# Kernel tuning notes

Measured on AMD Instinct MI355X. Metric: run time of the kernel, lower is better.

The kernel has to match this reference:

```python
import jax, jax.numpy as jnp
import numpy as np


def _apply_ring(x, angles):
    """Apply x @ R^T where R = G_0 @ G_1 @ ... @ G_{n-1} with ring planes
    (k, (k+1) % n). Equivalent to applying G_k^T to x for k = n-1 .. 0:
      x[:, k] <- c*x[:, k] - s*x[:, j]
      x[:, j] <- s*x[:, k] + c*x[:, j]
    x: [B, n], angles: [n].
    """
    n = angles.shape[0]

    def step(xT, k):
        a = angles[k]
        c, s = jnp.cos(a), jnp.sin(a)
        j = jnp.mod(k + 1, n)
        xi = xT[k]
        xj = xT[j]
        xT = xT.at[k].set(c * xi - s * xj)
        xT = xT.at[j].set(s * xi + c * xj)
        return xT, None

    ks = jnp.arange(n - 1, -1, -1)  # reverse order: R^T = G_{n-1}^T ... G_0^T
    xT, _ = jax.lax.scan(step, x.T, ks)  # carry is [n, B]
    return xT.T


def setup_inputs() -> dict:
    key = jax.random.key(0)
    k_x, k_e, k_d = jax.random.split(key, 3)
    B, n, num_blocks = 8192, 1024, 4
    return {
        "x": jax.random.normal(k_x, (B, n), dtype=jnp.float32),
        "angles_enc": jax.random.normal(k_e, (num_blocks, n), dtype=jnp.float32),
        "angles_dec": jax.random.normal(k_d, (num_blocks, n), dtype=jnp.float32),
        "hidden_weight": jnp.zeros((1,), dtype=jnp.float32),
        "hidden_state": jnp.zeros((n,), dtype=jnp.float32),
    }


def reference(x, angles_enc, angles_dec, hidden_weight, hidden_state):
    num_blocks = angles_enc.shape[0]
    b = x
    for blk in range(num_blocks):
        b = _apply_ring(b, angles_enc[blk])
    # recurrent blend; weight uses the detached hidden_weight (original uses
    # numpy on .detach()), so stop_gradient matches the original semantics.
    w = jax.nn.sigmoid(jax.lax.stop_gradient(hidden_weight[0]))
    bottleneck = (1.0 - w) * b + w * hidden_state[None, :]
    out = bottleneck
    for blk in range(num_blocks):
        out = _apply_ring(out, angles_dec[blk])
    return (bottleneck, out)
```

## Files before the change

### kernel.cpp

```cpp
#include <hip/hip_runtime.h>
#include <math.h>

#define N_COLS 1024
#define NRINGS 8

#define TPR    32
#define CHUNK  32
#define ROWS_PER_BLOCK 8

#define F_OFF   16384
#define A_OFF   24576
#define AUX_OFF 24832
#define WS_FLOATS 24848

__global__ void ced_setup(const float* __restrict__ ae,
                          const float* __restrict__ ad,
                          float* __restrict__ ws)
{
    __shared__ float2 ls[N_COLS];
    const int r   = blockIdx.x;
    const int tid = threadIdx.x;
    const float* ang = (r < 4) ? (ae + (r << 10)) : (ad + ((r - 4) << 10));

    #pragma unroll
    for (int m = 0; m < 4; ++m) {
        int k = tid * 4 + m;
        float sv, cv;
        sincosf(ang[k], &sv, &cv);
        if (k == N_COLS - 1) {
            ((float2*)(ws + AUX_OFF))[r] = make_float2(cv, sv);
            cv = 0.f; sv = -1.f;
        }
        ls[k] = make_float2(cv, sv);
    }
    __syncthreads();

    {
        int k0 = tid * 4;
        int t  = k0 >> 5;
        int jp = (k0 & 31) >> 1;
        float4* CS = (float4*)ws;
        float2 e0 = ls[k0], e1 = ls[k0+1], e2 = ls[k0+2], e3 = ls[k0+3];
        CS[(r*16 + jp    )*32 + t] = make_float4(e0.x, e0.y, e1.x, e1.y);
        CS[(r*16 + jp + 1)*32 + t] = make_float4(e2.x, e2.y, e3.x, e3.y);
    }

    if (tid < TPR) {
        int t = tid;
        float f[CHUNK];
        float P = 1.f;
        for (int j = CHUNK - 1; j >= 0; --j) {
            float2 cs = ls[t*CHUNK + j];
            f[j] = cs.x * P;
            P    = -cs.y * P;
        }
        float4* F = (float4*)(ws + F_OFF);
        #pragma unroll
        for (int qi = 0; qi < 8; ++qi)
            F[(r*8 + qi)*32 + t] = make_float4(f[4*qi], f[4*qi+1], f[4*qi+2], f[4*qi+3]);
        ws[A_OFF + r*TPR + t] = P;
    }
}

__global__ __launch_bounds__(256, 4)
void ced_main(const float* __restrict__ x,
              const float* __restrict__ ws,
              const float* __restrict__ hw,
              const float* __restrict__ hs,
              float* __restrict__ out, int B)
{
    const float4* CS  = (const float4*)ws;
    const float4* F   = (const float4*)(ws + F_OFF);
    const float*  A   = ws + A_OFF;
    const float2* AUX = (const float2*)(ws + AUX_OFF);

    const int tid  = threadIdx.x;
    const int lane = tid & 63;
    const int t    = lane & 31;
    const int g    = lane >> 5;
    const int groupBase = lane & 32;
    const int row  = blockIdx.x * ROWS_PER_BLOCK + (tid >> 6) * 2 + g;

    float y[CHUNK];
    const float4* xp = (const float4*)(x + (size_t)row * N_COLS + t * CHUNK);
    #pragma unroll
    for (int i = 0; i < 8; ++i) {
        float4 v = xp[i];
        y[4*i] = v.x; y[4*i+1] = v.y; y[4*i+2] = v.z; y[4*i+3] = v.w;
    }

    const float w   = 1.f / (1.f + expf(-hw[0]));
    const float omw = 1.f - w;

    #pragma unroll 1
    for (int r = 0; r < NRINGS; ++r) {
        if (r == 4) {
            float4* ob = (float4*)(out + (size_t)row * N_COLS + t * CHUNK);
            const float4* hp = (const float4*)(hs + t * CHUNK);
            #pragma unroll
            for (int i = 0; i < 8; ++i) {
                float4 h = hp[i];
                float4 bn;
                bn.x = fmaf(omw, y[4*i+0], w * h.x);
                bn.y = fmaf(omw, y[4*i+1], w * h.y);
                bn.z = fmaf(omw, y[4*i+2], w * h.z);
                bn.w = fmaf(omw, y[4*i+3], w * h.w);
                ob[i] = bn;
                y[4*i+0] = bn.x; y[4*i+1] = bn.y; y[4*i+2] = bn.z; y[4*i+3] = bn.w;
            }
        }

        const float2 cN = AUX[r];
        float y0 = __shfl(y[0],       groupBase);
        float yN = __shfl(y[CHUNK-1], groupBase + 31);
        float Cinit = cN.x * yN - cN.y * y0;
        float x0n   = fmaf(cN.y, yN, cN.x * y0);
        if (t == 0) y[0] = x0n;

        float carry = 0.f, ztmp = 0.f;
        const float4* csr = CS + r * 512 + t;
        #pragma unroll
        for (int jp = CHUNK/2 - 1; jp >= 0; --jp) {
            float4 cs4 = csr[jp * 32];
            const int j1 = 2*jp + 1;
            float z1 = fmaf(cs4.w, y[j1], cs4.z * carry);
            carry    = fmaf(-cs4.w, carry, cs4.z * y[j1]);
            if (j1 == CHUNK - 1) ztmp = z1; else y[j1+1] = z1;
            const int j0 = 2*jp;
            float z0s = fmaf(cs4.y, y[j0], cs4.x * carry);
            carry     = fmaf(-cs4.y, carry, cs4.x * y[j0]);
            y[j0+1] = z0s;
        }

        float sa = A[r*32 + t];
        float sb = carry;
        #pragma unroll
        for (int d = 1; d < TPR; d <<= 1) {
            float a2 = __shfl_down(sa, d);
            float b2 = __shfl_down(sb, d);
            if (t + d < TPR) { sb = fmaf(sa, b2, sb); sa *= a2; }
        }
        float ea = __shfl_down(sa, 1), eb = __shfl_down(sb, 1);
        float zfirst = fmaf(sa, Cinit, sb);
        float Cin = (t == TPR - 1) ? Cinit : fmaf(ea, Cinit, eb);

        const float4* fr = F + r * 256 + t;
        #pragma unroll
        for (int qi = CHUNK/4 - 1; qi >= 0; --qi) {
            float4 f4 = fr[qi * 32];
            const int j = 4*qi;
            if (j + 3 == CHUNK - 1) ztmp   = fmaf(f4.w, Cin, ztmp);
            else                    y[j+4] = fmaf(f4.w, Cin, y[j+4]);
            y[j+3] = fmaf(f4.z, Cin, y[j+3]);
            y[j+2] = fmaf(f4.y, Cin, y[j+2]);
            y[j+1] = fmaf(f4.x, Cin, y[j+1]);
        }

        float up = __shfl_up(ztmp, 1);
        y[0] = (t == 0) ? zfirst : up;
    }

    float4* oo = (float4*)(out + (size_t)B * N_COLS + (size_t)row * N_COLS + t * CHUNK);
    #pragma unroll
    for (int i = 0; i < 8; ++i)
        oo[i] = make_float4(y[4*i], y[4*i+1], y[4*i+2], y[4*i+3]);
}

__global__ __launch_bounds__(256, 2)
void ced_fallback(const float* __restrict__ x,
                  const float* __restrict__ ae,
                  const float* __restrict__ ad,
                  const float* __restrict__ hw,
                  const float* __restrict__ hs,
                  float* __restrict__ out, int B)
{
    __shared__ float2 s_cs[NRINGS * 64 * 16];
    __shared__ float  s_A [NRINGS * 16];
    __shared__ float2 s_aux[NRINGS];

    const int tid = threadIdx.x;
    for (int i = 0; i < 32; ++i) {
        int idx = i * 256 + tid;
        int r   = idx >> 10;
        int k   = idx & 1023;
        const float* ang = (r < 4) ? (ae + (r << 10)) : (ad + ((r - 4) << 10));
        float sv, cv;
        sincosf(ang[k], &sv, &cv);
        int t = k >> 6, j = k & 63;
        float2 e = make_float2(cv, sv);
        if (k == 1023) { s_aux[r] = e; e = make_float2(0.f, -1.f); }
        s_cs[(r * 64 + j) * 16 + t] = e;
    }
    __syncthreads();
    if (tid < NRINGS * 16) {
        int r = tid >> 4, t = tid & 15;
        float p = 1.f;
        for (int j = 0; j < 64; ++j) p *= -s_cs[(r * 64 + j) * 16 + t].y;
        s_A[tid] = p;
    }
    __syncthreads();

    const int lane      = tid & 63;
    const int g         = lane >> 4;
    const int t         = lane & 15;
    const int groupBase = lane & 48;
    const int row       = blockIdx.x * 16 + (tid >> 6) * 4 + g;

    const float* xr = x + (size_t)row * N_COLS + t * 64;
    float y[64];
    #pragma unroll
    for (int i = 0; i < 16; ++i) {
        float4 v = ((const float4*)xr)[i];
        y[4*i] = v.x; y[4*i+1] = v.y; y[4*i+2] = v.z; y[4*i+3] = v.w;
    }
    const float w   = 1.f / (1.f + expf(-hw[0]));
    const float omw = 1.f - w;

    for (int r = 0; r < NRINGS; ++r) {
        if (r == 4) {
            float4* ob = (float4*)(out + (size_t)row * N_COLS + t * 64);
            const float4* hp = (const float4*)(hs + t * 64);
            #pragma unroll
            for (int i = 0; i < 16; ++i) {
                float4 h = hp[i];
                float4 bn;
                bn.x = fmaf(omw, y[4*i+0], w * h.x);
                bn.y = fmaf(omw, y[4*i+1], w * h.y);
                bn.z = fmaf(omw, y[4*i+2], w * h.z);
                bn.w = fmaf(omw, y[4*i+3], w * h.w);
                ob[i] = bn;
                y[4*i+0] = bn.x; y[4*i+1] = bn.y; y[4*i+2] = bn.z; y[4*i+3] = bn.w;
            }
        }
        const float2* csr = s_cs + r * 64 * 16;
        const float2  cN  = s_aux[r];
        float y0 = __shfl(y[0],  groupBase);
        float yN = __shfl(y[63], groupBase + 15);
        float Cinit = cN.x * yN - cN.y * y0;
        float x0n   = fmaf(cN.y, yN, cN.x * y0);
        if (t == 0) y[0] = x0n;

        float carry = 0.f, ztmp = 0.f;
        #pragma unroll
        for (int j = 63; j >= 0; --j) {
            float2 cs = csr[j * 16 + t];
            float z   = fmaf(cs.y, y[j], cs.x * carry);
            carry     = fmaf(-cs.y, carry, cs.x * y[j]);
            if (j == 63) ztmp = z; else y[j + 1] = z;
        }
        float sa = s_A[r * 16 + t], sb = carry;
        #pragma unroll
        for (int d = 1; d < 16; d <<= 1) {
            float a2 = __shfl_down(sa, d);
            float b2 = __shfl_down(sb, d);
            if (t + d < 16) { sb = fmaf(sa, b2, sb); sa *= a2; }
        }
        float ea = __shfl_down(sa, 1);
        float eb = __shfl_down(sb, 1);
        float z0  = fmaf(sa, Cinit, sb);
        float Cin = (t == 15) ? Cinit : fmaf(ea, Cinit, eb);

        float P = 1.f;
        #pragma unroll
        for (int j = 63; j >= 0; --j) {
            float2 cs = csr[j * 16 + t];
            float f = cs.x * P;
            P = -cs.y * P;
            if (j == 63) ztmp = fmaf(f, Cin, ztmp);
            else         y[j + 1] = fmaf(f, Cin, y[j + 1]);
        }
        float up = __shfl_up(ztmp, 1);
        y[0] = (t == 0) ? z0 : up;
    }

    float4* oo = (float4*)(out + (size_t)B * N_COLS + (size_t)row * N_COLS + t * 64);
    #pragma unroll
    for (int i = 0; i < 16; ++i)
        oo[i] = make_float4(y[4*i], y[4*i+1], y[4*i+2], y[4*i+3]);
}

extern "C" void kernel_launch(void* const* d_in, const int* in_sizes, int n_in,
                              void* d_out, int out_size, void* d_ws, size_t ws_size,
                              hipStream_t stream) {
    const float* x  = (const float*)d_in[0];
    const float* ae = (const float*)d_in[1];
    const float* ad = (const float*)d_in[2];
    const float* hw = (const float*)d_in[3];
    const float* hs = (const float*)d_in[4];
    float* out = (float*)d_out;
    const int B = in_sizes[0] / N_COLS;

    if (ws_size >= WS_FLOATS * sizeof(float)) {
        hipLaunchKernelGGL(ced_setup, dim3(NRINGS), dim3(256), 0, stream,
                           ae, ad, (float*)d_ws);
        hipLaunchKernelGGL(ced_main, dim3(B / ROWS_PER_BLOCK), dim3(256), 0, stream,
                           x, (const float*)d_ws, hw, hs, out, B);
    } else {
        hipLaunchKernelGGL(ced_fallback, dim3(B / 16), dim3(256), 0, stream,
                           x, ae, ad, hw, hs, out, B);
    }
}
```

Measured before the change: 137.3 us.

## Parallelize setup suffix-product scan and prefetch ring coefficients into registers

```diff
diff --git a/kernel.cpp b/kernel.cpp
--- a/kernel.cpp
+++ b/kernel.cpp
@@ -13,9 +13,10 @@
 #define AUX_OFF 24832
 #define WS_FLOATS 24848
 
-__global__ void ced_setup(const float* __restrict__ ae,
-                          const float* __restrict__ ad,
-                          float* __restrict__ ws)
+__global__ __launch_bounds__(256)
+void ced_setup(const float* __restrict__ ae,
+               const float* __restrict__ ad,
+               float* __restrict__ ws)
 {
     __shared__ float2 ls[N_COLS];
     const int r   = blockIdx.x;
@@ -24,7 +25,7 @@
 
     #pragma unroll
     for (int m = 0; m < 4; ++m) {
-        int k = tid * 4 + m;
+        int k = (m << 8) + tid;
         float sv, cv;
         sincosf(ang[k], &sv, &cv);
         if (k == N_COLS - 1) {
@@ -35,31 +36,33 @@
     }
     __syncthreads();
 
-    {
-        int k0 = tid * 4;
-        int t  = k0 >> 5;
-        int jp = (k0 & 31) >> 1;
-        float4* CS = (float4*)ws;
-        float2 e0 = ls[k0], e1 = ls[k0+1], e2 = ls[k0+2], e3 = ls[k0+3];
-        CS[(r*16 + jp    )*32 + t] = make_float4(e0.x, e0.y, e1.x, e1.y);
-        CS[(r*16 + jp + 1)*32 + t] = make_float4(e2.x, e2.y, e3.x, e3.y);
-    }
-
-    if (tid < TPR) {
-        int t = tid;
-        float f[CHUNK];
-        float P = 1.f;
-        for (int j = CHUNK - 1; j >= 0; --j) {
-            float2 cs = ls[t*CHUNK + j];
-            f[j] = cs.x * P;
-            P    = -cs.y * P;
-        }
-        float4* F = (float4*)(ws + F_OFF);
-        #pragma unroll
-        for (int qi = 0; qi < 8; ++qi)
-            F[(r*8 + qi)*32 + t] = make_float4(f[4*qi], f[4*qi+1], f[4*qi+2], f[4*qi+3]);
-        ws[A_OFF + r*TPR + t] = P;
-    }
+    const int t = tid >> 3;
+    const int q = tid & 7;
+    const int j0 = t * CHUNK + 4 * q;
+    float2 e0 = ls[j0], e1 = ls[j0+1], e2 = ls[j0+2], e3 = ls[j0+3];
+
+    float4* CSw = (float4*)ws;
+    CSw[(r*16 + 2*q    )*32 + t] = make_float4(e0.x, e0.y, e1.x, e1.y);
+    CSw[(r*16 + 2*q + 1)*32 + t] = make_float4(e2.x, e2.y, e3.x, e3.y);
+
+    float f3 = e3.x;       float P = -e3.y;
+    float f2 = e2.x * P;   P *= -e2.y;
+    float f1 = e1.x * P;   P *= -e1.y;
+    float f0 = e0.x * P;   P *= -e0.y;
+
+    float ip = P;
+    #pragma unroll
+    for (int d = 1; d < 8; d <<= 1) {
+        float tmp = __shfl_down(ip, d);
+        if (q + d < 8) ip *= tmp;
+    }
+    float ex = __shfl_down(ip, 1);
+    if (q == 7) ex = 1.f;
+    f0 *= ex; f1 *= ex; f2 *= ex; f3 *= ex;
+
+    float4* Fw = (float4*)(ws + F_OFF);
+    Fw[(r*8 + q)*32 + t] = make_float4(f0, f1, f2, f3);
+    if (q == 0) ws[A_OFF + r*TPR + t] = ip;
 }
 
 __global__ __launch_bounds__(256, 4)
@@ -110,6 +113,11 @@
             }
         }
 
+        const float4* csr = CS + r * 512 + t;
+        float4 cs_all[16];
+        #pragma unroll
+        for (int jp = 0; jp < 16; ++jp) cs_all[jp] = csr[jp * 32];
+
         const float2 cN = AUX[r];
         float y0 = __shfl(y[0],       groupBase);
         float yN = __shfl(y[CHUNK-1], groupBase + 31);
@@ -118,10 +126,9 @@
         if (t == 0) y[0] = x0n;
 
         float carry = 0.f, ztmp = 0.f;
-        const float4* csr = CS + r * 512 + t;
         #pragma unroll
         for (int jp = CHUNK/2 - 1; jp >= 0; --jp) {
-            float4 cs4 = csr[jp * 32];
+            float4 cs4 = cs_all[jp];
             const int j1 = 2*jp + 1;
             float z1 = fmaf(cs4.w, y[j1], cs4.z * carry);
             carry    = fmaf(-cs4.w, carry, cs4.z * y[j1]);
@@ -132,6 +139,11 @@
             y[j0+1] = z0s;
         }
 
+        const float4* fr = F + r * 256 + t;
+        float4 f_all[8];
+        #pragma unroll
+        for (int qi = 0; qi < 8; ++qi) f_all[qi] = fr[qi * 32];
+
         float sa = A[r*32 + t];
         float sb = carry;
         #pragma unroll
@@ -144,10 +156,9 @@
         float zfirst = fmaf(sa, Cinit, sb);
         float Cin = (t == TPR - 1) ? Cinit : fmaf(ea, Cinit, eb);
 
-        const float4* fr = F + r * 256 + t;
         #pragma unroll
         for (int qi = CHUNK/4 - 1; qi >= 0; --qi) {
-            float4 f4 = fr[qi * 32];
+            float4 f4 = f_all[qi];
             const int j = 4*qi;
             if (j + 3 == CHUNK - 1) ztmp   = fmaf(f4.w, Cin, ztmp);
             else                    y[j+4] = fmaf(f4.w, Cin, y[j+4]);
```

Result: no change. 137.5 us (+0.1%).
